# Kernel tuning notes

Measured on AMD Instinct MI355X. Metric: run time of the kernel, lower is better.

The kernel has to match this reference:

```python
import jax, jax.numpy as jnp
import numpy as np

D, NQ, BS, NL, NH, NP, DFF = 256, 900, 8, 4, 8, 4, 1024
HD = D // NH
SHAPES = np.array([[100, 100], [50, 50], [25, 25], [13, 13]], dtype=np.int64)  # (H, W) per level
LSTART = np.concatenate([[0], np.cumsum(SHAPES[:, 0] * SHAPES[:, 1])[:-1]]).astype(np.int64)
LMEM = int((SHAPES[:, 0] * SHAPES[:, 1]).sum())


def layer_norm(x, g, b, eps=1e-5):
    mu = x.mean(-1, keepdims=True)
    var = ((x - mu) ** 2).mean(-1, keepdims=True)
    return (x - mu) * jax.lax.rsqrt(var + eps) * g + b


def _forward(tgt, tgt_query_pos, tgt_reference_points, memory,
             in_proj_w, in_proj_b, out_proj_w, out_proj_b,
             samp_off_w, samp_off_b, attn_w_w, attn_w_b,
             value_proj_w, value_proj_b, output_proj_w, output_proj_b,
             lin1_w, lin1_b, lin2_w, lin2_b,
             norm1_g, norm1_b, norm2_g, norm2_b, norm3_g, norm3_b):
    # ---- self-attention (seq-first, torch nn.MultiheadAttention semantics) ----
    q = tgt + tgt_query_pos  # q = k = with_pos_embed(tgt, pos)
    Wq, Wk, Wv = jnp.split(in_proj_w, 3, 0)
    bq, bk, bv = jnp.split(in_proj_b, 3, 0)
    def heads(x):  # (nq, bs, d) -> (bs, nh, nq, hd)
        return x.reshape(NQ, BS, NH, HD).transpose(1, 2, 0, 3)
    qh = heads(q @ Wq.T + bq)
    kh = heads(q @ Wk.T + bk)
    vh = heads(tgt @ Wv.T + bv)
    attn = jax.nn.softmax(jnp.einsum('bhqd,bhkd->bhqk', qh, kh) / np.float32(np.sqrt(HD)), -1)
    sa = jnp.einsum('bhqk,bhkd->bhqd', attn, vh).transpose(2, 0, 1, 3).reshape(NQ, BS, D)
    sa = sa @ out_proj_w.T + out_proj_b
    t = layer_norm(tgt + sa, norm2_g, norm2_b)

    # ---- MSDeformAttn cross-attention (batch-first internally) ----
    qb = (t + tgt_query_pos).transpose(1, 0, 2)          # (bs, nq, d)
    refb = tgt_reference_points.transpose(1, 0, 2, 3)    # (bs, nq, nl, 2) in [0,1]
    memb = memory.transpose(1, 0, 2)                     # (bs, L, d)
    value = (memb @ value_proj_w.T + value_proj_b).reshape(BS, LMEM, NH, HD)
    off = (qb @ samp_off_w.T + samp_off_b).reshape(BS, NQ, NH, NL, NP, 2)
    aw = jax.nn.softmax((qb @ attn_w_w.T + attn_w_b).reshape(BS, NQ, NH, NL * NP), -1)
    aw = aw.reshape(BS, NQ, NH, NL, NP)
    normz = jnp.asarray(SHAPES[:, ::-1].copy(), dtype=jnp.float32)  # (nl, 2) = [W, H]
    loc = refb[:, :, None, :, None, :] + off / normz[None, None, None, :, None, :]

    out = jnp.zeros((BS, NQ, NH, HD), jnp.float32)
    for l in range(NL):  # fixed small number of pyramid levels
        Hl, Wl = int(SHAPES[l, 0]), int(SHAPES[l, 1])
        s = int(LSTART[l])
        v_l = value[:, s:s + Hl * Wl]  # (bs, Hl*Wl, nh, hd)
        # grid_sample(align_corners=False, padding=zeros) pixel coords
        x = (loc[:, :, :, l, :, 0] * Wl - 0.5).transpose(0, 1, 3, 2).reshape(BS, NQ * NP, NH)
        y = (loc[:, :, :, l, :, 1] * Hl - 0.5).transpose(0, 1, 3, 2).reshape(BS, NQ * NP, NH)
        x0 = jnp.floor(x)
        y0 = jnp.floor(y)
        samp = jnp.zeros((BS, NQ * NP, NH, HD), jnp.float32)
        for dx in (0, 1):
            for dy in (0, 1):
                xc = x0 + dx
                yc = y0 + dy
                w = (1.0 - jnp.abs(x - xc)) * (1.0 - jnp.abs(y - yc))
                valid = (xc >= 0) & (xc < Wl) & (yc >= 0) & (yc < Hl)
                idx = (jnp.clip(yc, 0, Hl - 1) * Wl + jnp.clip(xc, 0, Wl - 1)).astype(jnp.int32)
                g = jnp.take_along_axis(v_l, idx[..., None], axis=1)  # (bs, nq*np, nh, hd)
                samp = samp + jnp.where(valid, w, 0.0)[..., None] * g
        samp = samp.reshape(BS, NQ, NP, NH, HD)
        out = out + jnp.einsum('bqhp,bqphd->bqhd', aw[:, :, :, l], samp)
    ca = (out.reshape(BS, NQ, D) @ output_proj_w.T + output_proj_b).transpose(1, 0, 2)
    t = layer_norm(t + ca, norm1_g, norm1_b)

    # ---- FFN ----
    ffn = jax.nn.relu(t @ lin1_w.T + lin1_b) @ lin2_w.T + lin2_b
    return layer_norm(t + ffn, norm3_g, norm3_b)


def setup_inputs() -> dict:
    key = jax.random.key(0)
    ks = jax.random.split(key, 24)
    r = lambda i, shape, s: jax.random.normal(ks[i], shape, jnp.float32) * s
    return {
        'tgt': r(0, (NQ, BS, D), 1.0),
        'tgt_query_pos': r(1, (NQ, BS, D), 1.0),
        'tgt_reference_points': jax.random.uniform(ks[2], (NQ, BS, NL, 2), jnp.float32),
        'memory': r(3, (LMEM, BS, D), 1.0),
        'spatial_shapes': jnp.asarray(SHAPES),
        'level_start_index': jnp.asarray(LSTART),
        'in_proj_w': r(4, (3 * D, D), 0.02), 'in_proj_b': r(5, (3 * D,), 0.02),
        'out_proj_w': r(6, (D, D), 0.02), 'out_proj_b': r(7, (D,), 0.02),
        'samp_off_w': r(8, (NH * NL * NP * 2, D), 0.01), 'samp_off_b': r(9, (NH * NL * NP * 2,), 0.01),
        'attn_w_w': r(10, (NH * NL * NP, D), 0.02), 'attn_w_b': r(11, (NH * NL * NP,), 0.02),
        'value_proj_w': r(12, (D, D), 0.02), 'value_proj_b': r(13, (D,), 0.02),
        'output_proj_w': r(14, (D, D), 0.02), 'output_proj_b': r(15, (D,), 0.02),
        'lin1_w': r(16, (DFF, D), 0.02), 'lin1_b': r(17, (DFF,), 0.02),
        'lin2_w': r(18, (D, DFF), 0.02), 'lin2_b': r(19, (D,), 0.02),
        'norm1_g': jnp.ones((D,), jnp.float32), 'norm1_b': jnp.zeros((D,), jnp.float32),
        'norm2_g': jnp.ones((D,), jnp.float32), 'norm2_b': jnp.zeros((D,), jnp.float32),
        'norm3_g': jnp.ones((D,), jnp.float32), 'norm3_b': jnp.zeros((D,), jnp.float32),
    }


def reference(tgt, tgt_query_pos, tgt_reference_points, memory, spatial_shapes, level_start_index,
              in_proj_w, in_proj_b, out_proj_w, out_proj_b, samp_off_w, samp_off_b,
              attn_w_w, attn_w_b, value_proj_w, value_proj_b, output_proj_w, output_proj_b,
              lin1_w, lin1_b, lin2_w, lin2_b, norm1_g, norm1_b, norm2_g, norm2_b, norm3_g, norm3_b):
    # spatial_shapes / level_start_index are static level constants (module-level SHAPES/LSTART)
    return _forward(tgt, tgt_query_pos, tgt_reference_points, memory,
                    in_proj_w, in_proj_b, out_proj_w, out_proj_b,
                    samp_off_w, samp_off_b, attn_w_w, attn_w_b,
                    value_proj_w, value_proj_b, output_proj_w, output_proj_b,
                    lin1_w, lin1_b, lin2_w, lin2_b,
                    norm1_g, norm1_b, norm2_g, norm2_b, norm3_g, norm3_b)
```

## Files before the change

### kernel.cpp

```cpp
#include <hip/hip_runtime.h>
#include <hip/hip_bf16.h>


namespace {
constexpr int D_ = 256;
constexpr int NQ_ = 900;
constexpr int BS_ = 8;
constexpr int NH_ = 8;
constexpr int HD_ = 32;
constexpr int DFF_ = 1024;
constexpr int MTOK = NQ_ * BS_;
constexpr int LMEM_ = 13294;
constexpr long T = (long)MTOK * D_;
constexpr float QSC = 0.17677669529663687f;
constexpr int QKS = 512;
}

typedef __attribute__((ext_vector_type(8))) short bf8_t;
typedef __attribute__((ext_vector_type(4))) float f4_t;

#define MFMA16(a, b, c) __builtin_amdgcn_mfma_f32_16x16x32_bf16((a), (b), (c), 0, 0, 0)

__device__ __forceinline__ unsigned short bfbits(float x) {
    union { __hip_bfloat16 h; unsigned short u; } cv;
    cv.h = __float2bfloat16(x);
    return cv.u;
}
__device__ __forceinline__ float bf2f(unsigned short u) {
    union { float f; unsigned v; } cv;
    cv.v = ((unsigned)u) << 16;
    return cv.f;
}

__device__ __forceinline__ void gload16(const unsigned short* g, unsigned short* l) {
    __builtin_amdgcn_global_load_lds(
        (const __attribute__((address_space(1))) unsigned int*)(g),
        (__attribute__((address_space(3))) unsigned int*)(l), 16, 0, 0);
}
__device__ __forceinline__ void gload16f(const float* g, float* l) {
    __builtin_amdgcn_global_load_lds(
        (const __attribute__((address_space(1))) unsigned int*)(g),
        (__attribute__((address_space(3))) unsigned int*)(l), 16, 0, 0);
}

__global__ void conv_weights(
    const float* __restrict__ ipw, const float* __restrict__ opw,
    const float* __restrict__ sow, const float* __restrict__ aww,
    const float* __restrict__ vpw, const float* __restrict__ outpw,
    const float* __restrict__ l1w, const float* __restrict__ l2w,
    const float* __restrict__ ipb, const float* __restrict__ sob,
    const float* __restrict__ awb,
    unsigned short* __restrict__ Wbf, float* __restrict__ biasAll)
{
    if (blockIdx.x == 0) {
        for (int j = threadIdx.x; j < 512; j += 256)
            biasAll[j] = (j < 256) ? ipb[j] * QSC : ipb[j];
        for (int j = threadIdx.x; j < 384; j += 256)
            biasAll[512 + j] = (j < 256) ? sob[j] : awb[j - 256];
    }
    const long idx4 = (long)blockIdx.x * 256 + threadIdx.x;
    if (idx4 >= 253952) return;
    const long e = idx4 * 4;
    const float* src; long off; float sc = 1.f;
    if (e < 196608)      { src = ipw;   off = 0;      if (e < 65536) sc = QSC; }
    else if (e < 262144) { src = opw;   off = 196608; }
    else if (e < 327680) { src = sow;   off = 262144; }
    else if (e < 360448) { src = aww;   off = 327680; }
    else if (e < 425984) { src = vpw;   off = 360448; }
    else if (e < 491520) { src = outpw; off = 425984; }
    else if (e < 753664) { src = l1w;   off = 491520; }
    else                 { src = l2w;   off = 753664; }
    const float4 v = *(const float4*)(src + (e - off));
    union { unsigned short u[4]; uint2 w; } pk;
    pk.u[0] = bfbits(v.x * sc); pk.u[1] = bfbits(v.y * sc);
    pk.u[2] = bfbits(v.z * sc); pk.u[3] = bfbits(v.w * sc);
    *(uint2*)(Wbf + e) = pk.w;
}

template<bool RELU, bool OUTBF16>
__global__ __launch_bounds__(256) void gemm_mfma(
    const unsigned short* __restrict__ A, const unsigned short* __restrict__ W,
    const float* __restrict__ bias, void* __restrict__ C, int M, int N, int K)
{
    __shared__ unsigned short As[128 * 32];
    __shared__ unsigned short Ws[128 * 32];
    const int t = threadIdx.x;
    const long m0 = (long)blockIdx.x * 128;
    const int n0 = blockIdx.y * 128;
    const int row0 = t >> 2;
    const int cgp = (t & 3) ^ ((t >> 2) & 3);
    long ar0 = m0 + row0;        if (ar0 > M - 1) ar0 = M - 1;
    long ar1 = m0 + 64 + row0;   if (ar1 > M - 1) ar1 = M - 1;
    const unsigned short* ga0 = A + ar0 * K + cgp * 8;
    const unsigned short* ga1 = A + ar1 * K + cgp * 8;
    const unsigned short* gw0 = W + (long)(n0 + row0) * K + cgp * 8;
    const unsigned short* gw1 = W + (long)(n0 + 64 + row0) * K + cgp * 8;
    const int lane = t & 63, wave = t >> 6;
    const int c = lane & 15, g = lane >> 4;
    const int wr = wave >> 1, wc = wave & 1;
    const int sws = (g * 8) ^ ((c & 3) * 8);
    f4_t acc[4][4];
#pragma unroll
    for (int i = 0; i < 4; ++i)
#pragma unroll
        for (int j = 0; j < 4; ++j)
            acc[i][j] = f4_t{0.f, 0.f, 0.f, 0.f};

    for (int kb = 0; kb < K; kb += 32) {
        gload16(ga0 + kb, As + t * 8);
        gload16(ga1 + kb, As + 2048 + t * 8);
        gload16(gw0 + kb, Ws + t * 8);
        gload16(gw1 + kb, Ws + 2048 + t * 8);
        __syncthreads();
        bf8_t af[4], bfr[4];
#pragma unroll
        for (int i = 0; i < 4; ++i) {
            af[i] = *(const bf8_t*)(As + (wr * 64 + i * 16 + c) * 32 + sws);
            bfr[i] = *(const bf8_t*)(Ws + (wc * 64 + i * 16 + c) * 32 + sws);
        }
#pragma unroll
        for (int i = 0; i < 4; ++i)
#pragma unroll
            for (int j = 0; j < 4; ++j)
                acc[i][j] = MFMA16(af[i], bfr[j], acc[i][j]);
        __syncthreads();
    }

#pragma unroll
    for (int i = 0; i < 4; ++i) {
        const long rbase = m0 + wr * 64 + i * 16 + 4 * g;
#pragma unroll
        for (int j = 0; j < 4; ++j) {
            const int col = n0 + wc * 64 + j * 16 + c;
            const float bv = bias[col];
#pragma unroll
            for (int r = 0; r < 4; ++r) {
                const long rr = rbase + r;
                if (rr < M) {
                    float v = acc[i][j][r] + bv;
                    if (RELU) v = fmaxf(v, 0.f);
                    if (OUTBF16) ((unsigned short*)C)[rr * N + col] = bfbits(v);
                    else         ((float*)C)[rr * N + col] = v;
                }
            }
        }
    }
}

template<bool OUTBF16>
__global__ __launch_bounds__(256) void gemm_f32d(
    const float* __restrict__ A, const unsigned short* __restrict__ W,
    const float* __restrict__ bias, void* __restrict__ C,
    int M, int N, int K, int R1, int S1, int S2)
{
    __shared__ float Asf[64 * 32];
    __shared__ unsigned short Ws[128 * 32];
    const int t = threadIdx.x;
    const long m0 = (long)blockIdx.x * 64;
    const int n0 = blockIdx.y * 128;
    const int spA = (t & 7) ^ ((t >> 3) & 7);
    const float *gA0, *gA1;
    {
        int r0 = (int)m0 + 0  + (t >> 3); if (r0 > M - 1) r0 = M - 1;
        int r1 = (int)m0 + 32 + (t >> 3); if (r1 > M - 1) r1 = M - 1;
        gA0 = A + ((long)(r0 / R1) * S1 + (long)(r0 % R1) * S2) * K + spA * 4;
        gA1 = A + ((long)(r1 / R1) * S1 + (long)(r1 % R1) * S2) * K + spA * 4;
    }
    const int row0 = t >> 2;
    const int cgp = (t & 3) ^ ((t >> 2) & 3);
    const unsigned short* gw0 = W + (long)(n0 + row0) * K + cgp * 8;
    const unsigned short* gw1 = W + (long)(n0 + 64 + row0) * K + cgp * 8;
    const int lane = t & 63, wave = t >> 6;
    const int c = lane & 15, g = lane >> 4;
    const int wr = wave >> 1, wc = wave & 1;
    const int s0 = (2 * g) ^ (c & 7);
    const int s1 = (2 * g + 1) ^ (c & 7);
    const int sws = (g * 8) ^ ((c & 3) * 8);
    f4_t acc[2][4];
#pragma unroll
    for (int i = 0; i < 2; ++i)
#pragma unroll
        for (int j = 0; j < 4; ++j)
            acc[i][j] = f4_t{0.f, 0.f, 0.f, 0.f};

    for (int kb = 0; kb < K; kb += 32) {
        gload16f(gA0 + kb, Asf + t * 4);
        gload16f(gA1 + kb, Asf + 1024 + t * 4);
        gload16(gw0 + kb, Ws + t * 8);
        gload16(gw1 + kb, Ws + 2048 + t * 8);
        __syncthreads();
        bf8_t af[2], bfr[4];
#pragma unroll
        for (int i = 0; i < 2; ++i) {
            const int row = wr * 32 + i * 16 + c;
            const f4_t lo = *(const f4_t*)(Asf + row * 32 + s0 * 4);
            const f4_t hi = *(const f4_t*)(Asf + row * 32 + s1 * 4);
            union { bf8_t v; unsigned short u[8]; } pk;
            pk.u[0] = bfbits(lo[0]); pk.u[1] = bfbits(lo[1]);
            pk.u[2] = bfbits(lo[2]); pk.u[3] = bfbits(lo[3]);
            pk.u[4] = bfbits(hi[0]); pk.u[5] = bfbits(hi[1]);
            pk.u[6] = bfbits(hi[2]); pk.u[7] = bfbits(hi[3]);
            af[i] = pk.v;
        }
#pragma unroll
        for (int j = 0; j < 4; ++j)
            bfr[j] = *(const bf8_t*)(Ws + (wc * 64 + j * 16 + c) * 32 + sws);
#pragma unroll
        for (int i = 0; i < 2; ++i)
#pragma unroll
            for (int j = 0; j < 4; ++j)
                acc[i][j] = MFMA16(af[i], bfr[j], acc[i][j]);
        __syncthreads();
    }

#pragma unroll
    for (int i = 0; i < 2; ++i) {
        const long rbase = m0 + wr * 32 + i * 16 + 4 * g;
#pragma unroll
        for (int j = 0; j < 4; ++j) {
            const int col = n0 + wc * 64 + j * 16 + c;
            const float bv = bias[col];
#pragma unroll
            for (int r = 0; r < 4; ++r) {
                const long rr = rbase + r;
                if (rr < M) {
                    float v = acc[i][j][r] + bv;
                    if (OUTBF16) ((unsigned short*)C)[rr * N + col] = bfbits(v);
                    else         ((float*)C)[rr * N + col] = v;
                }
            }
        }
    }
}

template<bool OUTBF16>
__global__ __launch_bounds__(256) void gemm_f32a(
    const float* __restrict__ A, const float* __restrict__ A2,
    const unsigned short* __restrict__ W, const float* __restrict__ bias,
    void* __restrict__ C, int M, int N, int K)
{
    __shared__ unsigned short As[128 * 32];
    __shared__ unsigned short Ws[128 * 32];
    const int t = threadIdx.x;
    const long m0 = (long)blockIdx.x * 128;
    const int n0 = blockIdx.y * 128;
    const int row0 = t >> 2, cg = t & 3;
    const int cgp = cg ^ ((t >> 2) & 3);
    long ar0 = m0 + row0;        if (ar0 > M - 1) ar0 = M - 1;
    long ar1 = m0 + 64 + row0;   if (ar1 > M - 1) ar1 = M - 1;
    const float* Ap0 = A + ar0 * K + cg * 8;
    const float* Ap1 = A + ar1 * K + cg * 8;
    const float* Bp0 = A2 + ar0 * K + cg * 8;
    const float* Bp1 = A2 + ar1 * K + cg * 8;
    const unsigned short* gw0 = W + (long)(n0 + row0) * K + cgp * 8;
    const unsigned short* gw1 = W + (long)(n0 + 64 + row0) * K + cgp * 8;
    unsigned short* la0 = As + row0 * 32 + ((cg * 8) ^ ((row0 & 3) * 8));
    unsigned short* la1 = la0 + 2048;
    const int lane = t & 63, wave = t >> 6;
    const int c = lane & 15, g = lane >> 4;
    const int wr = wave >> 1, wc = wave & 1;
    const int sws = (g * 8) ^ ((c & 3) * 8);
    f4_t acc[4][4];
#pragma unroll
    for (int i = 0; i < 4; ++i)
#pragma unroll
        for (int j = 0; j < 4; ++j)
            acc[i][j] = f4_t{0.f, 0.f, 0.f, 0.f};

    for (int kb = 0; kb < K; kb += 32) {
        gload16(gw0 + kb, Ws + t * 8);
        gload16(gw1 + kb, Ws + 2048 + t * 8);
        const float4 a00 = *(const float4*)(Ap0 + kb);
        const float4 a01 = *(const float4*)(Ap0 + kb + 4);
        const float4 a10 = *(const float4*)(Ap1 + kb);
        const float4 a11 = *(const float4*)(Ap1 + kb + 4);
        const float4 b00 = *(const float4*)(Bp0 + kb);
        const float4 b01 = *(const float4*)(Bp0 + kb + 4);
        const float4 b10 = *(const float4*)(Bp1 + kb);
        const float4 b11 = *(const float4*)(Bp1 + kb + 4);
        union { bf8_t v; unsigned short u[8]; } p0, p1;
        p0.u[0] = bfbits(a00.x + b00.x); p0.u[1] = bfbits(a00.y + b00.y);
        p0.u[2] = bfbits(a00.z + b00.z); p0.u[3] = bfbits(a00.w + b00.w);
        p0.u[4] = bfbits(a01.x + b01.x); p0.u[5] = bfbits(a01.y + b01.y);
        p0.u[6] = bfbits(a01.z + b01.z); p0.u[7] = bfbits(a01.w + b01.w);
        p1.u[0] = bfbits(a10.x + b10.x); p1.u[1] = bfbits(a10.y + b10.y);
        p1.u[2] = bfbits(a10.z + b10.z); p1.u[3] = bfbits(a10.w + b10.w);
        p1.u[4] = bfbits(a11.x + b11.x); p1.u[5] = bfbits(a11.y + b11.y);
        p1.u[6] = bfbits(a11.z + b11.z); p1.u[7] = bfbits(a11.w + b11.w);
        *(bf8_t*)la0 = p0.v;
        *(bf8_t*)la1 = p1.v;
        __syncthreads();
        bf8_t af[4], bfr[4];
#pragma unroll
        for (int i = 0; i < 4; ++i) {
            af[i] = *(const bf8_t*)(As + (wr * 64 + i * 16 + c) * 32 + sws);
            bfr[i] = *(const bf8_t*)(Ws + (wc * 64 + i * 16 + c) * 32 + sws);
        }
#pragma unroll
        for (int i = 0; i < 4; ++i)
#pragma unroll
            for (int j = 0; j < 4; ++j)
                acc[i][j] = MFMA16(af[i], bfr[j], acc[i][j]);
        __syncthreads();
    }

#pragma unroll
    for (int i = 0; i < 4; ++i) {
        const long rbase = m0 + wr * 64 + i * 16 + 4 * g;
#pragma unroll
        for (int j = 0; j < 4; ++j) {
            const int col = n0 + wc * 64 + j * 16 + c;
            const float bv = bias[col];
#pragma unroll
            for (int r = 0; r < 4; ++r) {
                const long rr = rbase + r;
                if (rr < M) {
                    float v = acc[i][j][r] + bv;
                    if (OUTBF16) ((unsigned short*)C)[rr * N + col] = bfbits(v);
                    else         ((float*)C)[rr * N + col] = v;
                }
            }
        }
    }
}

__global__ __launch_bounds__(256) void attn_mfma(
    const unsigned short* __restrict__ Qb, const unsigned short* __restrict__ Kb,
    const unsigned short* __restrict__ Vb, unsigned short* __restrict__ sa)
{
    __shared__ float smemf[2112];
    unsigned short* Ks = (unsigned short*)smemf;
    unsigned short* Vt = (unsigned short*)(smemf + 1024);
    const int t = threadIdx.x;
    const int wave = t >> 6, lane = t & 63;
    const int g = lane >> 4, c = lane & 15;
    const int b = blockIdx.x >> 3, h = blockIdx.x & 7;
    const int q0 = blockIdx.y * 64 + wave * 16;
    const int q = q0 + c;
    const bool qv = q < NQ_;
    const bf8_t qf = *(const bf8_t*)(Qb + ((long)(qv ? q : 0) * BS_ + b) * QKS + h * HD_ + 8 * g);

    f4_t acc0 = {0.f, 0.f, 0.f, 0.f}, acc1 = {0.f, 0.f, 0.f, 0.f};
    float m_run = -1e30f, l_run = 0.f;
    const int sk = t >> 2, sd = (t & 3) * 8;

    for (int kc = 0; kc < NQ_; kc += 64) {
        __syncthreads();
        {
            const int key = kc + sk;
            union { bf8_t v; unsigned short u[8]; } kv, vv;
            if (key < NQ_) {
                kv.v = *(const bf8_t*)(Kb + ((long)key * BS_ + b) * QKS + h * HD_ + sd);
                vv.v = *(const bf8_t*)(Vb + ((long)key * BS_ + b) * D_ + h * HD_ + sd);
            } else {
#pragma unroll
                for (int u = 0; u < 8; ++u) { kv.u[u] = 0; vv.u[u] = 0; }
            }
            *(bf8_t*)(Ks + sk * 32 + sd) = kv.v;
#pragma unroll
            for (int u = 0; u < 8; ++u) {
                const int r = sd + u;
                Vt[r * 64 + (sk ^ ((r & 7) << 3))] = vv.u[u];
            }
        }
        __syncthreads();

        f4_t s[4];
#pragma unroll
        for (int tt = 0; tt < 4; ++tt) {
            const bf8_t kf = *(const bf8_t*)(Ks + (tt * 16 + c) * 32 + 8 * g);
            f4_t z = {0.f, 0.f, 0.f, 0.f};
            s[tt] = MFMA16(kf, qf, z);
        }
        float sv[16];
#pragma unroll
        for (int tt = 0; tt < 4; ++tt)
#pragma unroll
            for (int r = 0; r < 4; ++r) {
                float x = s[tt][r];
                if (kc + tt * 16 + 4 * g + r >= NQ_) x = -1e30f;
                sv[tt * 4 + r] = x;
            }
        float mloc = sv[0];
#pragma unroll
        for (int i = 1; i < 16; ++i) mloc = fmaxf(mloc, sv[i]);
        mloc = fmaxf(mloc, __shfl_xor(mloc, 16));
        mloc = fmaxf(mloc, __shfl_xor(mloc, 32));
        const float mnew = fmaxf(m_run, mloc);
        const float resc = __expf(m_run - mnew);
        float p[16], ls = 0.f;
#pragma unroll
        for (int i = 0; i < 16; ++i) { p[i] = __expf(sv[i] - mnew); ls += p[i]; }
        ls += __shfl_xor(ls, 16);
        ls += __shfl_xor(ls, 32);
        l_run = l_run * resc + ls;
        m_run = mnew;
#pragma unroll
        for (int r = 0; r < 4; ++r) { acc0[r] *= resc; acc1[r] *= resc; }

        unsigned pk[4][2];
#pragma unroll
        for (int tt = 0; tt < 4; ++tt) {
            pk[tt][0] = (unsigned)bfbits(p[tt * 4 + 0]) | ((unsigned)bfbits(p[tt * 4 + 1]) << 16);
            pk[tt][1] = (unsigned)bfbits(p[tt * 4 + 2]) | ((unsigned)bfbits(p[tt * 4 + 3]) << 16);
        }
        const int srcA = ((g & 1) << 5) + c;
        const int srcB = srcA + 16;
#pragma unroll
        for (int kh = 0; kh < 2; ++kh) {
            const unsigned a0 = __shfl(pk[kh * 2][0], srcA), b0_ = __shfl(pk[kh * 2 + 1][0], srcA);
            const unsigned a1 = __shfl(pk[kh * 2][1], srcA), b1_ = __shfl(pk[kh * 2 + 1][1], srcA);
            const unsigned a2 = __shfl(pk[kh * 2][0], srcB), b2_ = __shfl(pk[kh * 2 + 1][0], srcB);
            const unsigned a3 = __shfl(pk[kh * 2][1], srcB), b3_ = __shfl(pk[kh * 2 + 1][1], srcB);
            union { bf8_t v; unsigned u[4]; } pf;
            const bool hi = (g & 2);
            pf.u[0] = hi ? b0_ : a0; pf.u[1] = hi ? b1_ : a1;
            pf.u[2] = hi ? b2_ : a2; pf.u[3] = hi ? b3_ : a3;
            const int kcol = (kh * 32 + 8 * g) ^ ((c & 7) << 3);
            const bf8_t vf0 = *(const bf8_t*)(Vt + c * 64 + kcol);
            const bf8_t vf1 = *(const bf8_t*)(Vt + (16 + c) * 64 + kcol);
            acc0 = MFMA16(vf0, pf.v, acc0);
            acc1 = MFMA16(vf1, pf.v, acc1);
        }
    }

    __syncthreads();
    const float invl = 1.f / l_run;
    float* O = smemf + wave * 528;
#pragma unroll
    for (int r = 0; r < 4; ++r) {
        O[c * 33 + 4 * g + r] = acc0[r] * invl;
        O[c * 33 + 16 + 4 * g + r] = acc1[r] * invl;
    }
    __syncthreads();
    {
        const int ql = lane >> 2, part = lane & 3;
        const int qg = q0 + ql;
        if (qg < NQ_) {
            union { bf8_t v; unsigned short u[8]; } pk;
#pragma unroll
            for (int u = 0; u < 8; ++u) pk.u[u] = bfbits(O[ql * 33 + part * 8 + u]);
            *(bf8_t*)(sa + ((long)qg * BS_ + b) * D_ + h * HD_ + part * 8) = pk.v;
        }
    }
}

__global__ __launch_bounds__(256) void msdeform_kernel(
    const float* __restrict__ oa, const float* __restrict__ refp,
    const unsigned short* __restrict__ val, unsigned short* __restrict__ out)
{
    __shared__ float saw[128];
    __shared__ float redm[8], redi[8];
    __shared__ float swt[128][4];
    __shared__ int sidx[128][4];
    const int bq = blockIdx.x;
    const int b = bq / NQ_, q = bq % NQ_;
    const int t = threadIdx.x;
    if (t < 128) saw[t] = oa[(long)bq * 384 + 256 + t];
    __syncthreads();
    if (t < 8) {
        float mx = -1e30f;
        for (int i = 0; i < 16; ++i) mx = fmaxf(mx, saw[t * 16 + i]);
        float s = 0.f;
        for (int i = 0; i < 16; ++i) s += __expf(saw[t * 16 + i] - mx);
        redm[t] = mx; redi[t] = 1.f / s;
    }
    __syncthreads();
    if (t < 128) {
        const int h = t >> 4, lp = t & 15, l = lp >> 2, p = lp & 3;
        const float aw = __expf(saw[t] - redm[h]) * redi[h];
        const int Wi = (l == 0) ? 100 : (l == 1) ? 50 : (l == 2) ? 25 : 13;
        const int Hi = Wi;
        const int sl = (l == 0) ? 0 : (l == 1) ? 10000 : (l == 2) ? 12500 : 13125;
        const float offx = oa[(long)bq * 384 + h * 32 + l * 8 + p * 2 + 0];
        const float offy = oa[(long)bq * 384 + h * 32 + l * 8 + p * 2 + 1];
        const float refx = refp[(((long)q * BS_ + b) * 4 + l) * 2 + 0];
        const float refy = refp[(((long)q * BS_ + b) * 4 + l) * 2 + 1];
        const float fW = (float)Wi, fH = (float)Hi;
        const float x = (refx + offx / fW) * fW - 0.5f;
        const float y = (refy + offy / fH) * fH - 0.5f;
        const float x0f = floorf(x), y0f = floorf(y);
        const float fx = x - x0f, fy = y - y0f;
        const int ix = (int)x0f, iy = (int)y0f;
        const float wts[4] = {(1.f - fx) * (1.f - fy), fx * (1.f - fy),
                              (1.f - fx) * fy,          fx * fy};
        const int xs[4] = {ix, ix + 1, ix, ix + 1};
        const int ys[4] = {iy, iy, iy + 1, iy + 1};
#pragma unroll
        for (int tap = 0; tap < 4; ++tap) {
            const bool valid = (xs[tap] >= 0) & (xs[tap] < Wi) & (ys[tap] >= 0) & (ys[tap] < Hi);
            const int xc = min(max(xs[tap], 0), Wi - 1);
            const int yc = min(max(ys[tap], 0), Hi - 1);
            swt[t][tap] = valid ? aw * wts[tap] : 0.f;
            sidx[t][tap] = b * LMEM_ + sl + yc * Wi + xc;
        }
    }
    __syncthreads();
    const int h = t >> 5, r = t & 31, qd = r & 7, s = r >> 3;
    float a0 = 0.f, a1 = 0.f, a2 = 0.f, a3 = 0.f;
#pragma unroll
    for (int i = 0; i < 16; ++i) {
        const int j = h * 16 + i;
        const float wv = swt[j][s];
        const long base = (long)sidx[j][s] * D_ + h * HD_ + qd * 4;
        const uint2 raw = *(const uint2*)(val + base);
        a0 += wv * bf2f((unsigned short)(raw.x & 0xffff));
        a1 += wv * bf2f((unsigned short)(raw.x >> 16));
        a2 += wv * bf2f((unsigned short)(raw.y & 0xffff));
        a3 += wv * bf2f((unsigned short)(raw.y >> 16));
    }
    a0 += __shfl_xor(a0, 8); a0 += __shfl_xor(a0, 16);
    a1 += __shfl_xor(a1, 8); a1 += __shfl_xor(a1, 16);
    a2 += __shfl_xor(a2, 8); a2 += __shfl_xor(a2, 16);
    a3 += __shfl_xor(a3, 8); a3 += __shfl_xor(a3, 16);
    if (s == 0) {
        union { unsigned short u[4]; uint2 w; } pk;
        pk.u[0] = bfbits(a0); pk.u[1] = bfbits(a1); pk.u[2] = bfbits(a2); pk.u[3] = bfbits(a3);
        *(uint2*)(out + (long)bq * D_ + h * HD_ + qd * 4) = pk.w;
    }
}

__global__ __launch_bounds__(256) void ln_kernel(
    const float* __restrict__ inA, const float* __restrict__ inB,
    const float* __restrict__ g, const float* __restrict__ be,
    float* __restrict__ out, const float* __restrict__ pos,
    unsigned short* __restrict__ bfOut, int swapB, int bfMode)
{
    const int r = blockIdx.x * 4 + (threadIdx.x >> 6);
    const int lane = threadIdx.x & 63;
    long rb = r;
    if (swapB) rb = (long)(r & 7) * NQ_ + (r >> 3);
    const float4 a4 = *(const float4*)(inA + (long)r * D_ + lane * 4);
    const float4 b4 = *(const float4*)(inB + rb * D_ + lane * 4);
    float x[4] = {a4.x + b4.x, a4.y + b4.y, a4.z + b4.z, a4.w + b4.w};
    float s = x[0] + x[1] + x[2] + x[3];
#pragma unroll
    for (int off = 32; off > 0; off >>= 1) s += __shfl_xor(s, off);
    const float mu = s * (1.f / D_);
    float v = 0.f;
#pragma unroll
    for (int cc = 0; cc < 4; ++cc) { const float dd = x[cc] - mu; v += dd * dd; }
#pragma unroll
    for (int off = 32; off > 0; off >>= 1) v += __shfl_xor(v, off);
    const float rs = rsqrtf(v * (1.f / D_) + 1e-5f);
    const float4 g4 = *(const float4*)(g + lane * 4);
    const float4 e4 = *(const float4*)(be + lane * 4);
    const float gg[4] = {g4.x, g4.y, g4.z, g4.w};
    const float ee[4] = {e4.x, e4.y, e4.z, e4.w};
    float y[4];
#pragma unroll
    for (int cc = 0; cc < 4; ++cc) y[cc] = (x[cc] - mu) * rs * gg[cc] + ee[cc];
    *(float4*)(out + (long)r * D_ + lane * 4) = make_float4(y[0], y[1], y[2], y[3]);
    if (bfMode) {
        float z[4] = {y[0], y[1], y[2], y[3]};
        long er = r;
        if (bfMode == 2) {
            const float4 p4 = *(const float4*)(pos + (long)r * D_ + lane * 4);
            z[0] += p4.x; z[1] += p4.y; z[2] += p4.z; z[3] += p4.w;
            er = (long)(r & 7) * NQ_ + (r >> 3);
        }
        union { unsigned short u[4]; uint2 w; } pk;
        pk.u[0] = bfbits(z[0]); pk.u[1] = bfbits(z[1]);
        pk.u[2] = bfbits(z[2]); pk.u[3] = bfbits(z[3]);
        *(uint2*)(bfOut + er * D_ + lane * 4) = pk.w;
    }
}

extern "C" void kernel_launch(void* const* d_in, const int* in_sizes, int n_in,
                              void* d_out, int out_size, void* d_ws, size_t ws_size,
                              hipStream_t stream) {
    const float* tgt   = (const float*)d_in[0];
    const float* pos   = (const float*)d_in[1];
    const float* refp  = (const float*)d_in[2];
    const float* mem   = (const float*)d_in[3];
    const float* ipw   = (const float*)d_in[6];
    const float* ipb   = (const float*)d_in[7];
    const float* opw   = (const float*)d_in[8];
    const float* opb   = (const float*)d_in[9];
    const float* sow   = (const float*)d_in[10];
    const float* sob   = (const float*)d_in[11];
    const float* aww   = (const float*)d_in[12];
    const float* awb   = (const float*)d_in[13];
    const float* vpw   = (const float*)d_in[14];
    const float* vpb   = (const float*)d_in[15];
    const float* outpw = (const float*)d_in[16];
    const float* outpb = (const float*)d_in[17];
    const float* l1w   = (const float*)d_in[18];
    const float* l1b   = (const float*)d_in[19];
    const float* l2w   = (const float*)d_in[20];
    const float* l2b   = (const float*)d_in[21];
    const float* n1g = (const float*)d_in[22]; const float* n1be = (const float*)d_in[23];
    const float* n2g = (const float*)d_in[24]; const float* n2be = (const float*)d_in[25];
    const float* n3g = (const float*)d_in[26]; const float* n3be = (const float*)d_in[27];

    char* wsb = (char*)d_ws;
    auto alloc = [&](size_t bytes) { char* p = wsb; wsb += (bytes + 255) & ~(size_t)255; return p; };
    unsigned short* Wbf       = (unsigned short*)alloc(1015808 * 2);
    float*          biasAll   = (float*)alloc(896 * 4);
    unsigned short* QK_bf     = (unsigned short*)alloc(T * 4);
    unsigned short* Vb_bf     = (unsigned short*)alloc(T * 2);
    unsigned short* sa_bf     = (unsigned short*)alloc(T * 2);
    float*          saproj    = (float*)alloc(T * 4);
    float*          t1        = (float*)alloc(T * 4);
    unsigned short* qplus2_bf = (unsigned short*)alloc(T * 2);
    float*          oa        = (float*)alloc((long)MTOK * 384 * 4);
    unsigned short* sampo_bf  = (unsigned short*)alloc(T * 2);
    float*          ca        = (float*)alloc(T * 4);
    float*          t2        = (float*)alloc(T * 4);
    unsigned short* t2_bf     = (unsigned short*)alloc(T * 2);
    unsigned short* ffnh_bf   = (unsigned short*)alloc((long)MTOK * DFF_ * 2);
    float*          ffno      = (float*)alloc(T * 4);
    unsigned short* val       = (unsigned short*)alloc((long)BS_ * LMEM_ * D_ * 2);
    const unsigned short* wqk   = Wbf + 0;
    const unsigned short* wv    = Wbf + 131072;
    const unsigned short* wo    = Wbf + 196608;
    const unsigned short* wsoaw = Wbf + 262144;
    const unsigned short* wvp   = Wbf + 360448;
    const unsigned short* wop   = Wbf + 425984;
    const unsigned short* wl1   = Wbf + 491520;
    const unsigned short* wl2   = Wbf + 753664;
    const float* bias_qk = biasAll;
    const float* bias_oa = biasAll + 512;

    const dim3 blk(256);
    const dim3 g_m(57, 2);

    conv_weights<<<992, blk, 0, stream>>>(ipw, opw, sow, aww, vpw, outpw, l1w, l2w,
                                          ipb, sob, awb, Wbf, biasAll);
    gemm_f32a<true><<<dim3(57, 4), blk, 0, stream>>>(tgt, pos, wqk, bias_qk, QK_bf,
                                                     MTOK, QKS, D_);
    gemm_f32d<true><<<dim3(113, 2), blk, 0, stream>>>(tgt, wv, ipb + 2 * D_, Vb_bf,
                                                      MTOK, D_, D_, MTOK, 0, 1);
    attn_mfma<<<dim3(64, 15), blk, 0, stream>>>(QK_bf, QK_bf + 256, Vb_bf, sa_bf);
    gemm_mfma<false, false><<<g_m, blk, 0, stream>>>(sa_bf, wo, opb, saproj, MTOK, D_, D_);
    ln_kernel<<<1800, blk, 0, stream>>>(tgt, saproj, n2g, n2be, t1, pos, qplus2_bf, 0, 2);
    gemm_f32d<true><<<dim3(1662, 2), blk, 0, stream>>>(mem, wvp, vpb, val,
                                                       BS_ * LMEM_, D_, D_, LMEM_, 1, BS_);
    gemm_mfma<false, false><<<dim3(57, 3), blk, 0, stream>>>(qplus2_bf, wsoaw, bias_oa, oa, MTOK, 384, D_);
    msdeform_kernel<<<7200, blk, 0, stream>>>(oa, refp, val, sampo_bf);
    gemm_mfma<false, false><<<g_m, blk, 0, stream>>>(sampo_bf, wop, outpb, ca, MTOK, D_, D_);
    ln_kernel<<<1800, blk, 0, stream>>>(t1, ca, n1g, n1be, t2, nullptr, t2_bf, 1, 1);
    gemm_mfma<true, true><<<dim3(57, 8), blk, 0, stream>>>(t2_bf, wl1, l1b, ffnh_bf, MTOK, DFF_, D_);
    gemm_mfma<false, false><<<g_m, blk, 0, stream>>>(ffnh_bf, wl2, l2b, ffno, MTOK, D_, DFF_);
    ln_kernel<<<1800, blk, 0, stream>>>(t2, ffno, n3g, n3be, (float*)d_out, nullptr, nullptr, 0, 0);
}
```

Measured before the change: 256.8 us.

## Keep value-projection weight tile resident in LDS with persistent row loop

Adds a persistent GEMM kernel for the large memory value projection. Each block loads its 128x256 bf16 weight slice into LDS once, with an XOR swizzle, then walks many 64-row tiles. A operands are read directly from global fp32 and converted to bf16 in registers, which removes per-tile weight reloads and the A staging through LDS. The cost is 64KB of LDS per block, which limits occupancy, and uncoalesced direct A loads without double buffering, so latency may be exposed.

Result: slower. 277.3 us (+8.0%).

```diff
diff --git a/kernel.cpp b/kernel.cpp
--- a/kernel.cpp
+++ b/kernel.cpp
@@ -145,6 +145,97 @@
             }
         }
     }
+}
+
+template<bool OUTBF16>
+__global__ __launch_bounds__(256) void gemm_wres(
+    const float* __restrict__ A, const unsigned short* __restrict__ W,
+    const float* __restrict__ bias, void* __restrict__ C,
+    int M, int N, int nTiles, int R1, int S1, int S2)
+{
+    __shared__ unsigned short Wl[128 * 256];
+    const int t = threadIdx.x;
+    const int n0 = blockIdx.y * 128;
+    {
+        const int rsub = t >> 5;
+        const int slot = t & 31;
+#pragma unroll
+        for (int i = 0; i < 16; ++i) {
+            const int r = i * 8 + rsub;
+            const int cg = slot ^ (r & 31);
+            gload16(W + (long)(n0 + r) * 256 + cg * 8, Wl + i * 2048 + t * 8);
+        }
+    }
+    __syncthreads();
+
+    const int lane = t & 63, wave = t >> 6;
+    const int c = lane & 15, g = lane >> 4;
+    const int wr = wave >> 1, wc = wave & 1;
+    int woff[4];
+#pragma unroll
+    for (int j = 0; j < 4; ++j) {
+        const int row = wc * 64 + j * 16 + c;
+        woff[j] = row * 256 + ((g ^ (row & 31)) * 8);
+    }
+
+    for (int mt = blockIdx.x; mt < nTiles; mt += gridDim.x) {
+        const long m0 = (long)mt * 64;
+        int gr0 = (int)m0 + wr * 32 + c;       if (gr0 > M - 1) gr0 = M - 1;
+        int gr1 = gr0 + 16;                    if (gr1 > M - 1) gr1 = M - 1;
+        const float* pA0 = A + ((long)(gr0 / R1) * S1 + (long)(gr0 % R1) * S2) * 256 + g * 8;
+        const float* pA1 = A + ((long)(gr1 / R1) * S1 + (long)(gr1 % R1) * S2) * 256 + g * 8;
+        f4_t acc[2][4];
+#pragma unroll
+        for (int i = 0; i < 2; ++i)
+#pragma unroll
+            for (int j = 0; j < 4; ++j)
+                acc[i][j] = f4_t{0.f, 0.f, 0.f, 0.f};
+
+#pragma unroll
+        for (int kb = 0; kb < 8; ++kb) {
+            const float4 l0 = *(const float4*)(pA0 + kb * 32);
+            const float4 h0 = *(const float4*)(pA0 + kb * 32 + 4);
+            const float4 l1 = *(const float4*)(pA1 + kb * 32);
+            const float4 h1 = *(const float4*)(pA1 + kb * 32 + 4);
+            union { bf8_t v; unsigned short u[8]; } p0, p1;
+            p0.u[0] = bfbits(l0.x); p0.u[1] = bfbits(l0.y); p0.u[2] = bfbits(l0.z); p0.u[3] = bfbits(l0.w);
+            p0.u[4] = bfbits(h0.x); p0.u[5] = bfbits(h0.y); p0.u[6] = bfbits(h0.z); p0.u[7] = bfbits(h0.w);
+            p1.u[0] = bfbits(l1.x); p1.u[1] = bfbits(l1.y); p1.u[2] = bfbits(l1.z); p1.u[3] = bfbits(l1.w);
+            p1.u[4] = bfbits(h1.x); p1.u[5] = bfbits(h1.y); p1.u[6] = bfbits(h1.z); p1.u[7] = bfbits(h1.w);
+            bf8_t bfr[4];
+#pragma unroll
+            for (int j = 0; j < 4; ++j) {
+                const int row = wc * 64 + j * 16 + c;
+                const int slot = (kb * 4 + g) ^ (row & 31);
+                bfr[j] = *(const bf8_t*)(Wl + row * 256 + slot * 8);
+            }
+#pragma unroll
+            for (int j = 0; j < 4; ++j) {
+                acc[0][j] = MFMA16(p0.v, bfr[j], acc[0][j]);
+                acc[1][j] = MFMA16(p1.v, bfr[j], acc[1][j]);
+            }
+        }
+
+#pragma unroll
+        for (int i = 0; i < 2; ++i) {
+            const long rbase = m0 + wr * 32 + i * 16 + 4 * g;
+#pragma unroll
+            for (int j = 0; j < 4; ++j) {
+                const int col = n0 + wc * 64 + j * 16 + c;
+                const float bv = bias[col];
+#pragma unroll
+                for (int r = 0; r < 4; ++r) {
+                    const long rr = rbase + r;
+                    if (rr < M) {
+                        float v = acc[i][j][r] + bv;
+                        if (OUTBF16) ((unsigned short*)C)[rr * N + col] = bfbits(v);
+                        else         ((float*)C)[rr * N + col] = v;
+                    }
+                }
+            }
+        }
+    }
+    (void)woff;
 }
 
 template<bool OUTBF16>
@@ -634,8 +725,8 @@
     attn_mfma<<<dim3(64, 15), blk, 0, stream>>>(QK_bf, QK_bf + 256, Vb_bf, sa_bf);
     gemm_mfma<false, false><<<g_m, blk, 0, stream>>>(sa_bf, wo, opb, saproj, MTOK, D_, D_);
     ln_kernel<<<1800, blk, 0, stream>>>(tgt, saproj, n2g, n2be, t1, pos, qplus2_bf, 0, 2);
-    gemm_f32d<true><<<dim3(1662, 2), blk, 0, stream>>>(mem, wvp, vpb, val,
-                                                       BS_ * LMEM_, D_, D_, LMEM_, 1, BS_);
+    gemm_wres<true><<<dim3(256, 2), blk, 0, stream>>>(mem, wvp, vpb, val,
+                                                      BS_ * LMEM_, D_, 1662, LMEM_, 1, BS_);
     gemm_mfma<false, false><<<dim3(57, 3), blk, 0, stream>>>(qplus2_bf, wsoaw, bias_oa, oa, MTOK, 384, D_);
     msdeform_kernel<<<7200, blk, 0, stream>>>(oa, refp, val, sampo_bf);
     gemm_mfma<false, false><<<g_m, blk, 0, stream>>>(sampo_bf, wop, outpb, ca, MTOK, D_, D_);
```
